# Performance work log

Hardware: AMD Instinct MI355X
Metric: run time of the kernel (lower is better)

Reference implementation:

```python
import jax, jax.numpy as jnp
import numpy as np

EPS_BN = 1e-5
EPS_NORM = 1e-12
TOP_K = 512


def _conv(x, w):
    # NCHW conv, stride 1, SAME padding (ultralytics Conv autopad)
    return jax.lax.conv_general_dilated(x, w, (1, 1), 'SAME',
                                        dimension_numbers=('NCHW', 'OIHW', 'NCHW'))


def _bn(x, g, b, m, v):
    # inference-mode BatchNorm2d
    inv = jax.lax.rsqrt(v + EPS_BN)
    return (x - m[None, :, None, None]) * (g * inv)[None, :, None, None] + b[None, :, None, None]


def _descriptor(feat, p):
    (w_dr, g_dr, b_dr, m_dr, v_dr,
     w_d1, g_d1, b_d1, m_d1, v_d1,
     g_e, b_e, m_e, v_e,
     w_d2, g_d2, b_d2, m_d2, v_d2) = p
    # dim_reduce: Conv(channel, channel//2, 1) = conv+BN+SiLU
    x = jax.nn.silu(_bn(_conv(feat, w_dr), g_dr, b_dr, m_dr, v_dr))
    # descriptor: Conv(c/2, c/2, 3) + BN + ReLU + Conv(c/2, c/4, 1)
    x = jax.nn.silu(_bn(_conv(x, w_d1), g_d1, b_d1, m_d1, v_d1))
    x = jax.nn.relu(_bn(x, g_e, b_e, m_e, v_e))
    x = jax.nn.silu(_bn(_conv(x, w_d2), g_d2, b_d2, m_d2, v_d2))
    return x


def _keypoints(desc):
    b, c, h, w = desc.shape
    resp = jnp.sqrt(jnp.sum(desc * desc, axis=1)).reshape(b, h * w)  # L2 norm over channels
    _, idx = jax.lax.top_k(resp, TOP_K)                              # [b, K]
    y = (idx // w).astype(desc.dtype) / (h - 1) * 2 - 1
    x = (idx % w).astype(desc.dtype) / (w - 1) * 2 - 1
    return jnp.stack([x, y], axis=-1), idx                           # [b,K,2], [b,K]


def _forward(rgb_feat, ir_feat, params):
    rgb_desc = _descriptor(rgb_feat, params)
    ir_desc = _descriptor(ir_feat, params)

    kp1, idx1 = _keypoints(rgb_desc)
    kp2, idx2 = _keypoints(ir_desc)

    b, c, h, w = rgb_desc.shape
    hw = h * w
    d1 = rgb_desc.reshape(b, c, hw)
    d2 = ir_desc.reshape(b, c, hw)
    d1 = d1 / jnp.maximum(jnp.linalg.norm(d1, axis=1, keepdims=True), EPS_NORM)
    d2 = d2 / jnp.maximum(jnp.linalg.norm(d2, axis=1, keepdims=True), EPS_NORM)
    corr = jnp.einsum('bcn,bcm->bnm', d1, d2)     # [b, hw, hw]
    soft = jax.nn.softmax(corr, axis=-1)

    # scalar matching weight per keypoint pair (gather at keypoint locations)
    bidx = jnp.arange(b)[:, None]
    wts = soft[bidx, idx1, idx2]                  # [b, K]

    # vectorized DLT: A rows, two per point, weighted
    x1, y1 = kp1[..., 0], kp1[..., 1]
    x2, y2 = kp2[..., 0], kp2[..., 1]
    one = jnp.ones_like(x1)
    zer = jnp.zeros_like(x1)
    r1 = jnp.stack([x1, y1, one, zer, zer, zer, -x2 * x1, -x2 * y1, -x2], axis=-1)
    r2 = jnp.stack([zer, zer, zer, x1, y1, one, -y2 * x1, -y2 * y1, -y2], axis=-1)
    A = jnp.stack([r1, r2], axis=2) * wts[:, :, None, None]   # [b,K,2,9]
    A = A.reshape(b, 2 * TOP_K, 9)

    _, _, Vh = jnp.linalg.svd(A, full_matrices=False)          # Vh: [b,9,9]
    # torch.svd returns V; original takes V[-1] == last COLUMN of jax Vh
    H = Vh[:, :, -1].reshape(b, 3, 3)
    return H, rgb_desc, ir_desc


def setup_inputs() -> dict:
    key = jax.random.key(0)
    ks = jax.random.split(key, 8)
    B, C, Hh, Ww = 2, 256, 64, 64
    c2, c4 = C // 2, C // 4
    f32 = jnp.float32

    def bn_params(c):
        return (jnp.ones((c,), f32), jnp.zeros((c,), f32),
                jnp.zeros((c,), f32), jnp.ones((c,), f32))

    g_dr, b_dr, m_dr, v_dr = bn_params(c2)
    g_d1, b_d1, m_d1, v_d1 = bn_params(c2)
    g_e, b_e, m_e, v_e = bn_params(c2)
    g_d2, b_d2, m_d2, v_d2 = bn_params(c4)

    return {
        'rgb_feat': jax.random.normal(ks[0], (B, C, Hh, Ww), f32),
        'ir_feat': jax.random.normal(ks[1], (B, C, Hh, Ww), f32),
        'w_dr': jax.random.normal(ks[2], (c2, C, 1, 1), f32) * 0.05,
        'g_dr': g_dr, 'b_dr': b_dr, 'm_dr': m_dr, 'v_dr': v_dr,
        'w_d1': jax.random.normal(ks[3], (c2, c2, 3, 3), f32) * 0.05,
        'g_d1': g_d1, 'b_d1': b_d1, 'm_d1': m_d1, 'v_d1': v_d1,
        'g_e': g_e, 'b_e': b_e, 'm_e': m_e, 'v_e': v_e,
        'w_d2': jax.random.normal(ks[4], (c4, c2, 1, 1), f32) * 0.05,
        'g_d2': g_d2, 'b_d2': b_d2, 'm_d2': m_d2, 'v_d2': v_d2,
    }


def reference(rgb_feat, ir_feat,
              w_dr, g_dr, b_dr, m_dr, v_dr,
              w_d1, g_d1, b_d1, m_d1, v_d1,
              g_e, b_e, m_e, v_e,
              w_d2, g_d2, b_d2, m_d2, v_d2):
    params = (w_dr, g_dr, b_dr, m_dr, v_dr,
              w_d1, g_d1, b_d1, m_d1, v_d1,
              g_e, b_e, m_e, v_e,
              w_d2, g_d2, b_d2, m_d2, v_d2)
    return _forward(rgb_feat, ir_feat, params)
```

## Files before the change

kernel.cpp:

```cpp
#include <hip/hip_runtime.h>
#include <math.h>


#define HW4 4096
#define NIMG 4

#define OFF_X1   0L
#define OFF_X2   (OFF_X1 + 4L*128*4096)
#define OFF_RESP (OFF_X2 + 4L*128*4096)
#define OFF_INVN (OFF_RESP + 4L*4096)
#define OFF_TOPI (OFF_INVN + 4L*4096)
#define OFF_WTS  (OFF_TOPI + 4L*512)
#define OFF_A    (OFF_WTS + 2L*512)
#define OFF_QN   OFF_X1
#define OFF_PART (OFF_X1 + 65536L)

#define NSPLIT 16

__device__ __forceinline__ float silu_f(float y) { return y / (1.f + expf(-y)); }

__global__ __launch_bounds__(256) void fm_conv1(
    const float* __restrict__ rgb, const float* __restrict__ ir,
    const float* __restrict__ w, const float* __restrict__ g,
    const float* __restrict__ bb, const float* __restrict__ mm,
    const float* __restrict__ vv, float* __restrict__ x1) {
  __shared__ float wl[256*8];
  int bid = blockIdx.x;
  int pblk = bid & 7, ocg = (bid >> 3) & 15, img = bid >> 7;
  int oc0 = ocg * 8;
  int tid = threadIdx.x;
  const float* src = (img < 2) ? (rgb + (long)img*256*HW4) : (ir + (long)(img-2)*256*HW4);
  for (int i = tid; i < 2048; i += 256) {
    int o = i & 7, ic = i >> 3;
    wl[i] = w[(oc0 + o)*256 + ic];
  }
  __syncthreads();
  int p0 = pblk*512 + tid*2;
  float acc[8][2];
  #pragma unroll
  for (int o = 0; o < 8; ++o) { acc[o][0] = 0.f; acc[o][1] = 0.f; }
  #pragma unroll 4
  for (int ic = 0; ic < 256; ++ic) {
    float2 v = *(const float2*)(src + (long)ic*HW4 + p0);
    float4 wa = *(const float4*)&wl[ic*8];
    float4 wb = *(const float4*)&wl[ic*8 + 4];
    acc[0][0] = fmaf(wa.x, v.x, acc[0][0]); acc[0][1] = fmaf(wa.x, v.y, acc[0][1]);
    acc[1][0] = fmaf(wa.y, v.x, acc[1][0]); acc[1][1] = fmaf(wa.y, v.y, acc[1][1]);
    acc[2][0] = fmaf(wa.z, v.x, acc[2][0]); acc[2][1] = fmaf(wa.z, v.y, acc[2][1]);
    acc[3][0] = fmaf(wa.w, v.x, acc[3][0]); acc[3][1] = fmaf(wa.w, v.y, acc[3][1]);
    acc[4][0] = fmaf(wb.x, v.x, acc[4][0]); acc[4][1] = fmaf(wb.x, v.y, acc[4][1]);
    acc[5][0] = fmaf(wb.y, v.x, acc[5][0]); acc[5][1] = fmaf(wb.y, v.y, acc[5][1]);
    acc[6][0] = fmaf(wb.z, v.x, acc[6][0]); acc[6][1] = fmaf(wb.z, v.y, acc[6][1]);
    acc[7][0] = fmaf(wb.w, v.x, acc[7][0]); acc[7][1] = fmaf(wb.w, v.y, acc[7][1]);
  }
  #pragma unroll
  for (int o = 0; o < 8; ++o) {
    int oc = oc0 + o;
    float inv = 1.f / sqrtf(vv[oc] + 1e-5f);
    float sc = g[oc]*inv;
    float2 r;
    r.x = silu_f((acc[o][0] - mm[oc])*sc + bb[oc]);
    r.y = silu_f((acc[o][1] - mm[oc])*sc + bb[oc]);
    *(float2*)(x1 + ((long)img*128 + oc)*HW4 + p0) = r;
  }
}

#define C3_TW 72
#define C3_TR 18
__global__ __launch_bounds__(256) void fm_conv3(
    const float* __restrict__ x1, const float* __restrict__ w,
    const float* __restrict__ g1, const float* __restrict__ b1,
    const float* __restrict__ m1, const float* __restrict__ v1,
    const float* __restrict__ ge, const float* __restrict__ be,
    const float* __restrict__ me, const float* __restrict__ ve,
    float* __restrict__ x2) {
  __shared__ float t[2][4][C3_TR*C3_TW];
  __shared__ float wl[2][4][9][4];
  int bid = blockIdx.x;
  int rt = bid & 3, ocg = (bid >> 2) & 31, img = bid >> 7;
  int oc0 = ocg * 4;
  int y0 = rt * 16;
  int tid = threadIdx.x;
  int ly = tid >> 4;
  int lx = tid & 15;
  int x0 = lx * 4;
  const float* xim = x1 + (long)img*128*HW4;

  int gbase[5][4];
  int lofs[5];
  #pragma unroll
  for (int t5 = 0; t5 < 5; ++t5) {
    int i = tid + 256*t5;
    if (i < 1224) {
      int q = i / 306, r = i - q*306;
      int row = r / 17, seg = r - row*17;
      int gy = y0 + row - 1;
      lofs[t5] = q*(C3_TR*C3_TW) + row*C3_TW + 4 + seg*4;
      #pragma unroll
      for (int e = 0; e < 4; ++e) {
        int x = seg*4 + e - 1;
        gbase[t5][e] = (gy >= 0 && gy < 64 && x >= 0 && x < 64)
                       ? (q*HW4 + gy*64 + x) : -1;
      }
    } else {
      lofs[t5] = -1;
      #pragma unroll
      for (int e = 0; e < 4; ++e) gbase[t5][e] = -1;
    }
  }
  int wg0 = -1, wl0 = 0;
  {
    int i = tid;
    if (i < 144) {
      int o = i & 3, k = (i >> 2) % 9, q = i / 36;
      wg0 = ((oc0 + o)*128 + q)*9 + k;
      wl0 = (q*9 + k)*4 + o;
    }
  }

  float4 sreg[5];
  float wreg0 = 0.f;

  #define C3_LOAD(IC0) do {                                              \
    long icoff = (long)(IC0)*HW4;                                        \
    _Pragma("unroll")                                                    \
    for (int t5 = 0; t5 < 5; ++t5) {                                     \
      sreg[t5].x = (gbase[t5][0] >= 0) ? xim[icoff + gbase[t5][0]] : 0.f;\
      sreg[t5].y = (gbase[t5][1] >= 0) ? xim[icoff + gbase[t5][1]] : 0.f;\
      sreg[t5].z = (gbase[t5][2] >= 0) ? xim[icoff + gbase[t5][2]] : 0.f;\
      sreg[t5].w = (gbase[t5][3] >= 0) ? xim[icoff + gbase[t5][3]] : 0.f;\
    }                                                                    \
    if (wg0 >= 0) wreg0 = w[(long)(IC0)*9 + wg0];                        \
  } while (0)

  #define C3_WRITE(BUF) do {                                             \
    float* tb = &t[BUF][0][0];                                           \
    _Pragma("unroll")                                                    \
    for (int t5 = 0; t5 < 5; ++t5)                                       \
      if (lofs[t5] >= 0) *(float4*)(tb + lofs[t5]) = sreg[t5];           \
    if (wg0 >= 0) (&wl[BUF][0][0][0])[wl0] = wreg0;                      \
  } while (0)

  float acc[4][4];
  #pragma unroll
  for (int o = 0; o < 4; ++o)
    #pragma unroll
    for (int j = 0; j < 4; ++j) acc[o][j] = 0.f;

  C3_LOAD(0);
  C3_WRITE(0);
  __syncthreads();
  int pb = 0;
  for (int ic0 = 0; ic0 < 128; ic0 += 4) {
    if (ic0 + 4 < 128) C3_LOAD(ic0 + 4);
    #pragma unroll
    for (int q = 0; q < 4; ++q) {
      const float* tq = &t[pb][q][0];
      float n6[3][6];
      #pragma unroll
      for (int dy = 0; dy < 3; ++dy) {
        float4 a = *(const float4*)(tq + (ly + dy)*C3_TW + x0 + 4);
        float4 b2 = *(const float4*)(tq + (ly + dy)*C3_TW + x0 + 8);
        n6[dy][0] = a.x; n6[dy][1] = a.y; n6[dy][2] = a.z;
        n6[dy][3] = a.w; n6[dy][4] = b2.x; n6[dy][5] = b2.y;
      }
      #pragma unroll
      for (int k = 0; k < 9; ++k) {
        const int dy = k / 3, dx = k % 3;
        float4 wA = *(const float4*)&wl[pb][q][k][0];
        #pragma unroll
        for (int j = 0; j < 4; ++j) {
          float nv = n6[dy][dx + j];
          acc[0][j] = fmaf(wA.x, nv, acc[0][j]);
          acc[1][j] = fmaf(wA.y, nv, acc[1][j]);
          acc[2][j] = fmaf(wA.z, nv, acc[2][j]);
          acc[3][j] = fmaf(wA.w, nv, acc[3][j]);
        }
      }
    }
    if (ic0 + 4 < 128) C3_WRITE(pb ^ 1);
    __syncthreads();
    pb ^= 1;
  }
  int prow = (y0 + ly)*64 + x0;
  #pragma unroll
  for (int o = 0; o < 4; ++o) {
    int oc = oc0 + o;
    float inv1 = 1.f / sqrtf(v1[oc] + 1e-5f);
    float s1 = g1[oc]*inv1;
    float inve = 1.f / sqrtf(ve[oc] + 1e-5f);
    float s2 = ge[oc]*inve;
    float4 r;
    float y;
    y = silu_f((acc[o][0] - m1[oc])*s1 + b1[oc]); r.x = fmaxf((y - me[oc])*s2 + be[oc], 0.f);
    y = silu_f((acc[o][1] - m1[oc])*s1 + b1[oc]); r.y = fmaxf((y - me[oc])*s2 + be[oc], 0.f);
    y = silu_f((acc[o][2] - m1[oc])*s1 + b1[oc]); r.z = fmaxf((y - me[oc])*s2 + be[oc], 0.f);
    y = silu_f((acc[o][3] - m1[oc])*s1 + b1[oc]); r.w = fmaxf((y - me[oc])*s2 + be[oc], 0.f);
    *(float4*)(x2 + ((long)img*128 + oc)*HW4 + prow) = r;
  }
}

__global__ __launch_bounds__(256) void fm_conv2(
    const float* __restrict__ x2, const float* __restrict__ w,
    const float* __restrict__ g, const float* __restrict__ bb,
    const float* __restrict__ mm, const float* __restrict__ vv,
    float* __restrict__ out) {
  __shared__ float wl[128*4];
  int bid = blockIdx.x;
  int pblk = bid & 7, ocg = (bid >> 3) & 15, img = bid >> 7;
  int oc0 = ocg * 4;
  int tid = threadIdx.x;
  for (int i = tid; i < 512; i += 256) {
    int o = i & 3, ic = i >> 2;
    wl[i] = w[(oc0 + o)*128 + ic];
  }
  __syncthreads();
  int p0 = pblk*512 + tid*2;
  const float* src = x2 + (long)img*128*HW4;
  float acc[4][2];
  #pragma unroll
  for (int o = 0; o < 4; ++o) { acc[o][0] = 0.f; acc[o][1] = 0.f; }
  #pragma unroll 4
  for (int ic = 0; ic < 128; ++ic) {
    float2 v = *(const float2*)(src + (long)ic*HW4 + p0);
    float4 wa = *(const float4*)&wl[ic*4];
    acc[0][0] = fmaf(wa.x, v.x, acc[0][0]); acc[0][1] = fmaf(wa.x, v.y, acc[0][1]);
    acc[1][0] = fmaf(wa.y, v.x, acc[1][0]); acc[1][1] = fmaf(wa.y, v.y, acc[1][1]);
    acc[2][0] = fmaf(wa.z, v.x, acc[2][0]); acc[2][1] = fmaf(wa.z, v.y, acc[2][1]);
    acc[3][0] = fmaf(wa.w, v.x, acc[3][0]); acc[3][1] = fmaf(wa.w, v.y, acc[3][1]);
  }
  #pragma unroll
  for (int o = 0; o < 4; ++o) {
    int oc = oc0 + o;
    float inv = 1.f / sqrtf(vv[oc] + 1e-5f);
    float sc = g[oc]*inv;
    float* dst = out + 18 + (long)img*262144 + (long)oc*HW4 + p0;
    dst[0] = silu_f((acc[o][0] - mm[oc])*sc + bb[oc]);
    dst[1] = silu_f((acc[o][1] - mm[oc])*sc + bb[oc]);
  }
}

__global__ __launch_bounds__(256) void fm_resp(
    const float* __restrict__ out, float* __restrict__ resp, float* __restrict__ invn) {
  int t = blockIdx.x*256 + threadIdx.x;
  if (t >= NIMG*HW4) return;
  int img = t >> 12, p = t & 4095;
  const float* d = out + 18 + (long)img*262144;
  float s = 0.f;
  #pragma unroll
  for (int c = 0; c < 64; ++c) { float x = d[c*HW4 + p]; s = fmaf(x, x, s); }
  float r = sqrtf(s);
  resp[t] = r;
  invn[t] = 1.f / fmaxf(r, 1e-12f);
}

__global__ __launch_bounds__(1024) void fm_sort(
    const float* __restrict__ resp, int* __restrict__ topidx) {
  __shared__ unsigned long long keys[4096];
  int img = blockIdx.x, tid = threadIdx.x;
  const float* r = resp + (long)img*HW4;
  for (int i = tid; i < 4096; i += 1024) {
    unsigned int vb = __float_as_uint(r[i]);
    keys[i] = ((unsigned long long)vb << 32) | (unsigned int)(4095 - i);
  }
  __syncthreads();
  for (int k = 2; k <= 4096; k <<= 1) {
    for (int j = k >> 1; j > 0; j >>= 1) {
      for (int t = tid; t < 2048; t += 1024) {
        int i = 2*t - (t & (j - 1));
        int ixj = i ^ j;
        bool up = ((i & k) == 0);
        unsigned long long a = keys[i], b = keys[ixj];
        if ((a < b) == up) { keys[i] = b; keys[ixj] = a; }
      }
      __syncthreads();
    }
  }
  if (tid < 512) topidx[img*512 + tid] = 4095 - (int)(keys[tid] & 0xFFFFFFFFull);
}

__global__ __launch_bounds__(256) void fm_qgather(
    const float* __restrict__ out, const float* __restrict__ invn,
    const int* __restrict__ topidx, float* __restrict__ qn) {
  int tid = threadIdx.x;
  int kp = blockIdx.x*4 + (tid >> 6);
  int c = tid & 63;
  int b = kp >> 9, k = kp & 511;
  int row = topidx[b*512 + k];
  const float* d1 = out + 18 + (long)b*262144;
  qn[(long)kp*64 + c] = d1[c*HW4 + row] * invn[(long)b*HW4 + row];
}

__global__ __launch_bounds__(256) void fm_corr(
    const float* __restrict__ out, const float* __restrict__ invn,
    const float* __restrict__ qn, float* __restrict__ part) {
  __shared__ float Qs[32*64];
  __shared__ float Ds[64*128];
  int tid = threadIdx.x;
  int tx = tid & 31, ty = tid >> 5;
  int jsplit = blockIdx.x;
  int kg = blockIdx.y;
  int b = blockIdx.z;
  int k0 = kg*32;
  const float* d2 = out + 18 + (long)(2 + b)*262144;
  const float* in2 = invn + (long)(2 + b)*HW4;
  {
    const float4* src = (const float4*)(qn + ((long)b*512 + k0)*64);
    float4* dst = (float4*)Qs;
    dst[tid] = src[tid];
    dst[tid + 256] = src[tid + 256];
  }
  float m[4], s[4];
  #pragma unroll
  for (int r = 0; r < 4; ++r) { m[r] = -INFINITY; s[r] = 0.f; }
  #pragma unroll
  for (int tile = 0; tile < 2; ++tile) {
    int j0 = jsplit*256 + tile*128;
    __syncthreads();
    {
      float4* dst = (float4*)Ds;
      #pragma unroll
      for (int t = 0; t < 8; ++t) {
        int i = tid + 256*t;
        int c = i >> 5, col4 = i & 31;
        dst[i] = *(const float4*)(d2 + (long)c*HW4 + j0 + col4*4);
      }
    }
    __syncthreads();
    float acc[4][4];
    #pragma unroll
    for (int r = 0; r < 4; ++r)
      #pragma unroll
      for (int cc = 0; cc < 4; ++cc) acc[r][cc] = 0.f;
    const float4* Ds4 = (const float4*)Ds;
    #pragma unroll 4
    for (int c = 0; c < 64; ++c) {
      float4 dv = Ds4[c*32 + tx];
      #pragma unroll
      for (int r = 0; r < 4; ++r) {
        float qv = Qs[(ty*4 + r)*64 + c];
        acc[r][0] = fmaf(qv, dv.x, acc[r][0]);
        acc[r][1] = fmaf(qv, dv.y, acc[r][1]);
        acc[r][2] = fmaf(qv, dv.z, acc[r][2]);
        acc[r][3] = fmaf(qv, dv.w, acc[r][3]);
      }
    }
    float i0 = in2[j0 + tx*4 + 0];
    float i1 = in2[j0 + tx*4 + 1];
    float i2 = in2[j0 + tx*4 + 2];
    float i3 = in2[j0 + tx*4 + 3];
    #pragma unroll
    for (int r = 0; r < 4; ++r) {
      float v0 = acc[r][0]*i0, v1 = acc[r][1]*i1, v2 = acc[r][2]*i2, v3 = acc[r][3]*i3;
      float vm = fmaxf(fmaxf(v0, v1), fmaxf(v2, v3));
      float nm = fmaxf(m[r], vm);
      s[r] = s[r]*expf(m[r] - nm) + expf(v0 - nm) + expf(v1 - nm) + expf(v2 - nm) + expf(v3 - nm);
      m[r] = nm;
    }
  }
  #pragma unroll
  for (int off = 1; off < 32; off <<= 1) {
    #pragma unroll
    for (int r = 0; r < 4; ++r) {
      float om = __shfl_xor(m[r], off);
      float os = __shfl_xor(s[r], off);
      float nm = fmaxf(m[r], om);
      s[r] = s[r]*expf(m[r] - nm) + os*expf(om - nm);
      m[r] = nm;
    }
  }
  if (tx == 0) {
    #pragma unroll
    for (int r = 0; r < 4; ++r) {
      long idx = (((long)b*512 + k0 + ty*4 + r)*NSPLIT + jsplit)*2;
      part[idx] = m[r];
      part[idx + 1] = s[r];
    }
  }
}

__global__ __launch_bounds__(256) void fm_comb(
    const float* __restrict__ out, const float* __restrict__ invn,
    const int* __restrict__ topidx, const float* __restrict__ qn,
    const float* __restrict__ part, float* __restrict__ wts) {
  int tid = threadIdx.x;
  int kp = blockIdx.x*4 + (tid >> 6);
  int lane = tid & 63;
  int b = kp >> 9, k = kp & 511;
  int col = topidx[(2 + b)*512 + k];
  const float* d2 = out + 18 + (long)(2 + b)*262144;
  float dot = qn[(long)kp*64 + lane] * d2[lane*HW4 + col];
  #pragma unroll
  for (int off = 1; off < 64; off <<= 1) dot += __shfl_xor(dot, off);
  if (lane == 0) {
    const float* pp = part + (long)kp*NSPLIT*2;
    float M = -INFINITY;
    #pragma unroll
    for (int i = 0; i < NSPLIT; ++i) M = fmaxf(M, pp[2*i]);
    float S = 0.f;
    #pragma unroll
    for (int i = 0; i < NSPLIT; ++i) S += pp[2*i + 1]*expf(pp[2*i] - M);
    float v = dot * invn[(long)(2 + b)*HW4 + col];
    wts[b*512 + k] = expf(v - M)/S;
  }
}

__global__ __launch_bounds__(256) void fm_build(
    const int* __restrict__ topidx, const float* __restrict__ wts,
    float* __restrict__ A) {
  int t = blockIdx.x*256 + threadIdx.x;
  if (t >= 1024) return;
  int b = t >> 9, k = t & 511;
  int i1 = topidx[b*512 + k], i2 = topidx[(2 + b)*512 + k];
  float w = wts[b*512 + k];
  float x1 = (float)(i1 & 63) / 63.f * 2.f - 1.f;
  float y1 = (float)(i1 >> 6) / 63.f * 2.f - 1.f;
  float x2 = (float)(i2 & 63) / 63.f * 2.f - 1.f;
  float y2 = (float)(i2 >> 6) / 63.f * 2.f - 1.f;
  float* r = A + ((long)b*1024 + 2*k)*9;
  r[0] = x1*w;  r[1] = y1*w;  r[2] = w;
  r[3] = 0.f;   r[4] = 0.f;   r[5] = 0.f;
  r[6] = (-x2*x1)*w; r[7] = (-x2*y1)*w; r[8] = (-x2)*w;
  r[9]  = 0.f;  r[10] = 0.f;  r[11] = 0.f;
  r[12] = x1*w; r[13] = y1*w; r[14] = w;
  r[15] = (-y2*x1)*w; r[16] = (-y2*y1)*w; r[17] = (-y2)*w;
}

__device__ __forceinline__ void lap_slartg(float f, float g, float* cs, float* sn, float* r) {
  if (g == 0.f) { *cs = 1.f; *sn = 0.f; *r = f; }
  else if (f == 0.f) { *cs = 0.f; *sn = copysignf(1.f, g); *r = fabsf(g); }
  else {
    float d = sqrtf(f*f + g*g);
    *cs = fabsf(f) / d;
    *r = copysignf(d, f);
    *sn = g / (*r);
  }
}

__device__ __forceinline__ void lap_slas2(float f, float g, float h, float* ssmin, float* ssmax) {
  float fa = fabsf(f), ga = fabsf(g), ha = fabsf(h);
  float fhmn = fminf(fa, ha), fhmx = fmaxf(fa, ha);
  if (fhmn == 0.f) {
    *ssmin = 0.f;
    if (fhmx == 0.f) *ssmax = ga;
    else {
      float mx = fmaxf(fhmx, ga), mn = fminf(fhmx, ga);
      float q = mn / mx;
      *ssmax = mx * sqrtf(1.f + q*q);
    }
  } else {
    if (ga < fhmx) {
      float as_ = 1.f + fhmn/fhmx;
      float at_ = (fhmx - fhmn)/fhmx;
      float au = ga/fhmx; au = au*au;
      float c = 2.f / (sqrtf(as_*as_ + au) + sqrtf(at_*at_ + au));
      *ssmin = fhmn*c;
      *ssmax = fhmx/c;
    } else {
      float au = fhmx/ga;
      if (au == 0.f) { *ssmin = (fhmn*fhmx)/ga; *ssmax = ga; }
      else {
        float as_ = 1.f + fhmn/fhmx;
        float at_ = (fhmx - fhmn)/fhmx;
        float t1 = as_*au, t2 = at_*au;
        float c = 1.f / (sqrtf(1.f + t1*t1) + sqrtf(1.f + t2*t2));
        float smn = (fhmn*c)*au;
        *ssmin = smn + smn;
        *ssmax = ga/(c + c);
      }
    }
  }
}

__device__ __forceinline__ void lap_slasv2(float f, float g, float h, float* ssmin, float* ssmax,
                           float* snr, float* csr, float* snl, float* csl) {
  const float epsv = 5.9604645e-08f;
  float ft = f, fa = fabsf(f), ht = h, ha = fabsf(h);
  int pmax = 1;
  bool swap_ = (ha > fa);
  if (swap_) { pmax = 3; float tmp = ft; ft = ht; ht = tmp; tmp = fa; fa = ha; ha = tmp; }
  float gt = g, ga = fabsf(gt);
  float clt = 0.f, crt = 0.f, slt = 0.f, srt = 0.f;
  if (ga == 0.f) { *ssmin = ha; *ssmax = fa; clt = 1.f; crt = 1.f; slt = 0.f; srt = 0.f; }
  else {
    bool gasmal = true;
    if (ga > fa) {
      pmax = 2;
      if ((fa/ga) < epsv) {
        gasmal = false;
        *ssmax = ga;
        if (ha > 1.f) *ssmin = fa/(ga/ha); else *ssmin = (fa/ga)*ha;
        clt = 1.f; slt = ht/gt; srt = 1.f; crt = ft/gt;
      }
    }
    if (gasmal) {
      float d = fa - ha, l;
      if (d == fa) l = 1.f; else l = d/fa;
      float m_ = gt/ft;
      float t = 2.f - l;
      float mm2 = m_*m_, tt = t*t;
      float s = sqrtf(tt + mm2);
      float r_ = (l == 0.f) ? fabsf(m_) : sqrtf(l*l + mm2);
      float a = 0.5f*(s + r_);
      *ssmin = ha/a;
      *ssmax = fa*a;
      if (mm2 == 0.f) {
        if (l == 0.f) t = copysignf(2.f, ft)*copysignf(1.f, gt);
        else t = gt/copysignf(d, ft) + m_/t;
      } else {
        t = (m_/(s + t) + m_/(r_ + l))*(1.f + a);
      }
      float l2 = sqrtf(t*t + 4.f);
      crt = 2.f/l2;
      srt = t/l2;
      clt = (crt + srt*m_)/a;
      slt = (ht/ft)*srt/a;
    }
  }
  if (swap_) { *csl = srt; *snl = crt; *csr = slt; *snr = clt; }
  else { *csl = clt; *snl = slt; *csr = crt; *snr = srt; }
  float tsign = 1.f;
  if (pmax == 1) tsign = copysignf(1.f, *csr)*copysignf(1.f, *csl)*copysignf(1.f, f);
  if (pmax == 2) tsign = copysignf(1.f, *snr)*copysignf(1.f, *csl)*copysignf(1.f, g);
  if (pmax == 3) tsign = copysignf(1.f, *snr)*copysignf(1.f, *snl)*copysignf(1.f, h);
  *ssmax = copysignf(*ssmax, tsign);
  *ssmin = copysignf(*ssmin, tsign*copysignf(1.f, f)*copysignf(1.f, h));
}

__device__ __forceinline__ float get9(const float (&a)[9], int idx) {
  float v = a[0];
#pragma unroll
  for (int i = 1; i < 9; ++i) if (idx == i) v = a[i];
  return v;
}
__device__ __forceinline__ void set9(float (&a)[9], int idx, float val) {
#pragma unroll
  for (int i = 0; i < 9; ++i) if (idx == i) a[i] = val;
}

__device__ __forceinline__ void bdsqr9_reg(float (&dd)[9], float (&ee)[9], float (&vt)[9]) {
  const float eps_ = 5.9604645e-08f;
  const float unfl_ = 1.17549435e-38f;
  const float tol_ = 10.f*eps_;
  float sminoa = fabsf(dd[0]);
  if (sminoa != 0.f) {
    float mu = sminoa;
    bool z = false;
#pragma unroll
    for (int i = 1; i < 9; ++i) {
      if (!z) {
        mu = fabsf(dd[i])*(mu/(mu + fabsf(ee[i-1])));
        sminoa = fminf(sminoa, mu);
        if (sminoa == 0.f) z = true;
      }
    }
  }
  sminoa = sminoa / 3.f;
  float thresh = fmaxf(tol_*sminoa, 486.f*unfl_);
  int m = 9, iter = 0, oldll = -1, oldm = -1, idir = 0;
  float sminl = 0.f;
  int guard = 0;
  while (guard++ < 2000) {
    if (m <= 1) break;
    if (iter > 486) break;
    float smax = fabsf(get9(dd, m-1));
    int ll = 0; bool split = false;
#pragma unroll
    for (int l2 = 8; l2 >= 1; --l2) {
      if (l2 <= m - 1 && !split) {
        float abss = fabsf(dd[l2-1]);
        float abse = fabsf(ee[l2-1]);
        if (abse <= thresh) { ll = l2; split = true; }
        else smax = fmaxf(smax, fmaxf(abss, abse));
      }
    }
    if (split) {
      set9(ee, ll-1, 0.f);
      if (ll == m - 1) { m = m - 1; continue; }
    } else ll = 0;
    ll = ll + 1;
    if (ll == m - 1) {
      float d1 = get9(dd, m-2), e1 = get9(ee, m-2), d2v = get9(dd, m-1);
      float sigmn, sigmx, sinr, cosr, sinl_, cosl_;
      lap_slasv2(d1, e1, d2v, &sigmn, &sigmx, &sinr, &cosr, &sinl_, &cosl_);
      set9(dd, m-2, sigmx); set9(ee, m-2, 0.f); set9(dd, m-1, sigmn);
      float xt = get9(vt, m-2), yt = get9(vt, m-1);
      set9(vt, m-2, cosr*xt + sinr*yt);
      set9(vt, m-1, cosr*yt - sinr*xt);
      m -= 2; continue;
    }
    if (ll > oldm || m < oldll)
      idir = (fabsf(get9(dd, ll-1)) >= fabsf(get9(dd, m-1))) ? 1 : 2;
    bool conv = false;
    if (idir == 1) {
      if (fabsf(get9(ee, m-2)) <= tol_*fabsf(get9(dd, m-1))) { set9(ee, m-2, 0.f); continue; }
      float mu = fabsf(get9(dd, ll-1));
      sminl = mu;
#pragma unroll
      for (int lll = 1; lll <= 8; ++lll) {
        if (lll >= ll && lll <= m - 1 && !conv) {
          if (fabsf(ee[lll-1]) <= tol_*mu) { ee[lll-1] = 0.f; conv = true; }
          else {
            mu = fabsf(dd[lll])*(mu/(mu + fabsf(ee[lll-1])));
            sminl = fminf(sminl, mu);
          }
        }
      }
    } else {
      if (fabsf(get9(ee, ll-1)) <= tol_*fabsf(get9(dd, ll-1))) { set9(ee, ll-1, 0.f); continue; }
      float mu = fabsf(get9(dd, m-1));
      sminl = mu;
#pragma unroll
      for (int lll = 8; lll >= 1; --lll) {
        if (lll <= m - 1 && lll >= ll && !conv) {
          if (fabsf(ee[lll-1]) <= tol_*mu) { ee[lll-1] = 0.f; conv = true; }
          else {
            mu = fabsf(dd[lll-1])*(mu/(mu + fabsf(ee[lll-1])));
            sminl = fminf(sminl, mu);
          }
        }
      }
    }
    if (conv) continue;
    oldll = ll; oldm = m;
    float shift = 0.f, rdum;
    if (!(9.f*tol_*(sminl/smax) <= fmaxf(eps_, 0.01f*tol_))) {
      float sll;
      if (idir == 1) { sll = fabsf(get9(dd, ll-1)); lap_slas2(get9(dd, m-2), get9(ee, m-2), get9(dd, m-1), &shift, &rdum); }
      else           { sll = fabsf(get9(dd, m-1));  lap_slas2(get9(dd, ll-1), get9(ee, ll-1), get9(dd, ll), &shift, &rdum); }
      if (sll > 0.f) { float q = shift/sll; if (q*q < eps_) shift = 0.f; }
    }
    iter += m - ll;
    if (shift == 0.f) {
      if (idir == 1) {
        float cs = 1.f, oldcs = 1.f, sn = 0.f, oldsn = 0.f, r;
#pragma unroll
        for (int i = 1; i <= 8; ++i) {
          if (i >= ll && i <= m - 1) {
            lap_slartg(dd[i-1]*cs, ee[i-1], &cs, &sn, &r);
            if (i >= 2 && i > ll) ee[i-2] = oldsn*r;
            float dn;
            lap_slartg(oldcs*r, dd[i]*sn, &oldcs, &oldsn, &dn);
            dd[i-1] = dn;
            float t = vt[i]; vt[i] = cs*t - sn*vt[i-1]; vt[i-1] = sn*t + cs*vt[i-1];
          }
        }
        float h2 = get9(dd, m-1)*cs;
        set9(dd, m-1, h2*oldcs);
        set9(ee, m-2, h2*oldsn);
        if (fabsf(get9(ee, m-2)) <= thresh) set9(ee, m-2, 0.f);
      } else {
        float cs = 1.f, oldcs = 1.f, sn = 0.f, oldsn = 0.f, r;
#pragma unroll
        for (int i = 9; i >= 2; --i) {
          if (i <= m && i >= ll + 1) {
            lap_slartg(dd[i-1]*cs, ee[i-2], &cs, &sn, &r);
            if (i < m) ee[i-1] = oldsn*r;
            float dn;
            lap_slartg(oldcs*r, dd[i-2]*sn, &oldcs, &oldsn, &dn);
            dd[i-1] = dn;
            float c2 = oldcs, s2 = -oldsn;
            float t = vt[i-1]; vt[i-1] = c2*t - s2*vt[i-2]; vt[i-2] = s2*t + c2*vt[i-2];
          }
        }
        float h2 = get9(dd, ll-1)*cs;
        set9(dd, ll-1, h2*oldcs);
        set9(ee, ll-1, h2*oldsn);
        if (fabsf(get9(ee, ll-1)) <= thresh) set9(ee, ll-1, 0.f);
      }
    } else {
      if (idir == 1) {
        float d0 = get9(dd, ll-1);
        float f2 = (fabsf(d0) - shift)*(copysignf(1.f, d0) + shift/d0);
        float g2 = get9(ee, ll-1);
#pragma unroll
        for (int i = 1; i <= 8; ++i) {
          if (i >= ll && i <= m - 1) {
            float cr, sr, cl, sl, r;
            lap_slartg(f2, g2, &cr, &sr, &r);
            if (i >= 2 && i > ll) ee[i-2] = r;
            f2 = cr*dd[i-1] + sr*ee[i-1];
            ee[i-1] = cr*ee[i-1] - sr*dd[i-1];
            g2 = sr*dd[i];
            dd[i] = cr*dd[i];
            lap_slartg(f2, g2, &cl, &sl, &r);
            dd[i-1] = r;
            f2 = cl*ee[i-1] + sl*dd[i];
            dd[i] = cl*dd[i] - sl*ee[i-1];
            if (i < m - 1) { g2 = sl*ee[i]; ee[i] = cl*ee[i]; }
            float t = vt[i]; vt[i] = cr*t - sr*vt[i-1]; vt[i-1] = sr*t + cr*vt[i-1];
          }
        }
        set9(ee, m-2, f2);
        if (fabsf(get9(ee, m-2)) <= thresh) set9(ee, m-2, 0.f);
      } else {
        float dm = get9(dd, m-1);
        float f2 = (fabsf(dm) - shift)*(copysignf(1.f, dm) + shift/dm);
        float g2 = get9(ee, m-2);
#pragma unroll
        for (int i = 9; i >= 2; --i) {
          if (i <= m && i >= ll + 1) {
            float cr, sr, cl, sl, r;
            lap_slartg(f2, g2, &cr, &sr, &r);
            if (i < m) ee[i-1] = r;
            f2 = cr*dd[i-1] + sr*ee[i-2];
            ee[i-2] = cr*ee[i-2] - sr*dd[i-1];
            g2 = sr*dd[i-2];
            dd[i-2] = cr*dd[i-2];
            lap_slartg(f2, g2, &cl, &sl, &r);
            dd[i-1] = r;
            f2 = cl*ee[i-2] + sl*dd[i-2];
            dd[i-2] = cl*dd[i-2] - sl*ee[i-2];
            if (i >= 3 && i > ll + 1) { g2 = sl*ee[i-3]; ee[i-3] = cl*ee[i-3]; }
            float c2 = cl, s2 = -sl;
            float t = vt[i-1]; vt[i-1] = c2*t - s2*vt[i-2]; vt[i-2] = s2*t + c2*vt[i-2];
          }
        }
        set9(ee, ll-1, f2);
        if (fabsf(get9(ee, ll-1)) <= thresh) set9(ee, ll-1, 0.f);
      }
    }
  }
#pragma unroll
  for (int i = 0; i < 9; ++i) {
    if (dd[i] < 0.f) { dd[i] = -dd[i]; vt[i] = -vt[i]; }
  }
#pragma unroll
  for (int i = 1; i <= 8; ++i) {
    int isub = 1; float smin2 = dd[0];
#pragma unroll
    for (int j = 2; j <= 9; ++j) {
      if (j <= 10 - i) {
        if (dd[j-1] <= smin2) { isub = j; smin2 = dd[j-1]; }
      }
    }
    const int tgt = 10 - i;
    if (isub != tgt) {
      set9(dd, isub-1, dd[tgt-1]);
      dd[tgt-1] = smin2;
      float tv = get9(vt, isub-1);
      set9(vt, isub-1, vt[tgt-1]);
      vt[tgt-1] = tv;
    }
  }
}

__global__ __launch_bounds__(256) void fm_svd(
    const float* __restrict__ Aglob, float* __restrict__ outH) {
  __shared__ float As[1024*9];
  __shared__ float wred[4][12];
  __shared__ float bc[4];
  int b = blockIdx.x, tid = threadIdx.x;
  int wv = tid >> 6, ln = tid & 63;
  const float* Ab = Aglob + (long)b*9216;
  {
    const float4* s4 = (const float4*)Ab;
    float4* d4 = (float4*)As;
#pragma unroll
    for (int t = 0; t < 9; ++t) d4[tid + 256*t] = s4[tid + 256*t];
  }
  __syncthreads();
  for (int k = 0; k < 9; ++k) {
    float ps = 0.f;
    for (int r = k + 1 + tid; r < 1024; r += 256) {
      float x = As[r*9 + k]; ps = fmaf(x, x, ps);
    }
#pragma unroll
    for (int off = 1; off < 64; off <<= 1) ps += __shfl_xor(ps, off);
    if (ln == 0) wred[wv][8] = ps;
    __syncthreads();
    if (tid == 0) {
      float ssq = wred[0][8] + wred[1][8] + wred[2][8] + wred[3][8];
      float alpha = As[k*9 + k];
      float tau = 0.f, sc = 0.f, beta = alpha;
      if (ssq != 0.f) {
        beta = -copysignf(sqrtf(alpha*alpha + ssq), alpha);
        tau = (beta - alpha)/beta;
        sc = 1.f/(alpha - beta);
      }
      bc[0] = tau; bc[1] = sc; bc[2] = beta;
    }
    __syncthreads();
    float tau = bc[0], sc = bc[1];
    if (tau != 0.f) {
      for (int r = k + 1 + tid; r < 1024; r += 256) As[r*9 + k] *= sc;
    }
    __syncthreads();
    if (tau != 0.f) {
      float pd[8];
#pragma unroll
      for (int jj = 0; jj < 8; ++jj) pd[jj] = 0.f;
      for (int r = k + 1 + tid; r < 1024; r += 256) {
        float vk = As[r*9 + k];
#pragma unroll
        for (int jj = 0; jj < 8; ++jj) {
          int j = k + 1 + jj;
          if (j < 9) pd[jj] = fmaf(vk, As[r*9 + j], pd[jj]);
        }
      }
#pragma unroll
      for (int off = 1; off < 64; off <<= 1) {
#pragma unroll
        for (int jj = 0; jj < 8; ++jj) pd[jj] += __shfl_xor(pd[jj], off);
      }
      if (ln == 0) {
#pragma unroll
        for (int jj = 0; jj < 8; ++jj) wred[wv][jj] = pd[jj];
      }
      __syncthreads();
      float sj[8];
#pragma unroll
      for (int jj = 0; jj < 8; ++jj) {
        int j = k + 1 + jj;
        float v = 0.f;
        if (j < 9)
          v = (wred[0][jj] + wred[1][jj] + wred[2][jj] + wred[3][jj] + As[k*9 + j]) * tau;
        sj[jj] = v;
      }
      for (int r = k + 1 + tid; r < 1024; r += 256) {
        float vk = As[r*9 + k];
#pragma unroll
        for (int jj = 0; jj < 8; ++jj) {
          int j = k + 1 + jj;
          if (j < 9) As[r*9 + j] -= sj[jj]*vk;
        }
      }
      __syncthreads();
      if (tid == 0) {
#pragma unroll
        for (int jj = 0; jj < 8; ++jj) {
          int j = k + 1 + jj;
          if (j < 9) As[k*9 + j] -= sj[jj];
        }
      }
    }
    if (tid == 0) As[k*9 + k] = bc[2];
    __syncthreads();
  }
  if (tid < 64) {
    float R[9][9];
#pragma unroll
    for (int i = 0; i < 9; ++i)
#pragma unroll
      for (int j = 0; j < 9; ++j)
        R[i][j] = (j >= i) ? As[i*9 + j] : 0.f;
    float dd[9], ee[9], taupv[8], pt8[9];
    ee[8] = 0.f;
#pragma unroll
    for (int i = 0; i < 9; ++i) {
      float alpha = R[i][i];
      float ssq = 0.f;
#pragma unroll
      for (int r2 = i + 1; r2 < 9; ++r2) ssq += R[r2][i]*R[r2][i];
      float tauq = 0.f, beta = alpha;
      if (ssq != 0.f) {
        beta = -copysignf(sqrtf(alpha*alpha + ssq), alpha);
        tauq = (beta - alpha)/beta;
        float scq = 1.f/(alpha - beta);
#pragma unroll
        for (int r2 = i + 1; r2 < 9; ++r2) R[r2][i] *= scq;
      }
      dd[i] = beta;
      if (tauq != 0.f) {
#pragma unroll
        for (int j = i + 1; j < 9; ++j) {
          float s = R[i][j];
#pragma unroll
          for (int r2 = i + 1; r2 < 9; ++r2) s += R[r2][i]*R[r2][j];
          s *= tauq;
          R[i][j] -= s;
#pragma unroll
          for (int r2 = i + 1; r2 < 9; ++r2) R[r2][j] -= s*R[r2][i];
        }
      }
      if (i < 8) {
        float alpha2 = R[i][i+1];
        float ssq2 = 0.f;
#pragma unroll
        for (int c = i + 2; c < 9; ++c) ssq2 += R[i][c]*R[i][c];
        float tp = 0.f, beta2 = alpha2;
        if (ssq2 != 0.f) {
          beta2 = -copysignf(sqrtf(alpha2*alpha2 + ssq2), alpha2);
          tp = (beta2 - alpha2)/beta2;
          float scp = 1.f/(alpha2 - beta2);
#pragma unroll
          for (int c = i + 2; c < 9; ++c) R[i][c] *= scp;
        }
        ee[i] = beta2;
        taupv[i] = tp;
        if (tp != 0.f) {
#pragma unroll
          for (int r2 = i + 1; r2 < 9; ++r2) {
            float s = R[r2][i+1];
#pragma unroll
            for (int c = i + 2; c < 9; ++c) s += R[i][c]*R[r2][c];
            s *= tp;
            R[r2][i+1] -= s;
#pragma unroll
            for (int c = i + 2; c < 9; ++c) R[r2][c] -= s*R[i][c];
          }
        }
      }
    }
#pragma unroll
    for (int i = 0; i < 9; ++i) pt8[i] = (i == 8) ? 1.f : 0.f;
#pragma unroll
    for (int i = 0; i < 8; ++i) {
      float tp = taupv[i];
      if (tp != 0.f) {
        float s = pt8[i+1];
#pragma unroll
        for (int r2 = i + 2; r2 < 9; ++r2) s += R[i][r2]*pt8[r2];
        s *= tp;
        pt8[i+1] -= s;
#pragma unroll
        for (int r2 = i + 2; r2 < 9; ++r2) pt8[r2] -= s*R[i][r2];
      }
    }
    float vt[9];
#pragma unroll
    for (int i = 0; i < 9; ++i) vt[i] = (i == tid) ? 1.f : 0.f;
    bdsqr9_reg(dd, ee, vt);
    float p8 = (tid < 9) ? get9(pt8, tid) : 0.f;
    float h[9];
#pragma unroll
    for (int i = 0; i < 9; ++i) h[i] = vt[i]*p8;
#pragma unroll
    for (int off = 1; off < 16; off <<= 1) {
#pragma unroll
      for (int i = 0; i < 9; ++i) h[i] += __shfl_xor(h[i], off);
    }
    if (tid == 0) {
#pragma unroll
      for (int i = 0; i < 9; ++i) outH[b*9 + i] = h[i];
    }
  }
}

extern "C" void kernel_launch(void* const* d_in, const int* in_sizes, int n_in,
                              void* d_out, int out_size, void* d_ws, size_t ws_size,
                              hipStream_t stream) {
  const float* rgb  = (const float*)d_in[0];
  const float* ir   = (const float*)d_in[1];
  const float* w_dr = (const float*)d_in[2];
  const float* g_dr = (const float*)d_in[3];
  const float* b_dr = (const float*)d_in[4];
  const float* m_dr = (const float*)d_in[5];
  const float* v_dr = (const float*)d_in[6];
  const float* w_d1 = (const float*)d_in[7];
  const float* g_d1 = (const float*)d_in[8];
  const float* b_d1 = (const float*)d_in[9];
  const float* m_d1 = (const float*)d_in[10];
  const float* v_d1 = (const float*)d_in[11];
  const float* g_e  = (const float*)d_in[12];
  const float* b_e  = (const float*)d_in[13];
  const float* m_e  = (const float*)d_in[14];
  const float* v_e  = (const float*)d_in[15];
  const float* w_d2 = (const float*)d_in[16];
  const float* g_d2 = (const float*)d_in[17];
  const float* b_d2 = (const float*)d_in[18];
  const float* m_d2 = (const float*)d_in[19];
  const float* v_d2 = (const float*)d_in[20];

  float* out = (float*)d_out;
  float* ws  = (float*)d_ws;
  float* x1   = ws + OFF_X1;
  float* x2   = ws + OFF_X2;
  float* resp = ws + OFF_RESP;
  float* invn = ws + OFF_INVN;
  int*   topi = (int*)(ws + OFF_TOPI);
  float* wts  = ws + OFF_WTS;
  float* Amat = ws + OFF_A;
  float* qn   = ws + OFF_QN;
  float* part = ws + OFF_PART;

  fm_conv1<<<512, 256, 0, stream>>>(rgb, ir, w_dr, g_dr, b_dr, m_dr, v_dr, x1);
  fm_conv3<<<512, 256, 0, stream>>>(x1, w_d1, g_d1, b_d1, m_d1, v_d1,
                                    g_e, b_e, m_e, v_e, x2);
  fm_conv2<<<512, 256, 0, stream>>>(x2, w_d2, g_d2, b_d2, m_d2, v_d2, out);
  fm_resp<<<(NIMG*HW4 + 255)/256, 256, 0, stream>>>(out, resp, invn);
  fm_sort<<<NIMG, 1024, 0, stream>>>(resp, topi);
  fm_qgather<<<256, 256, 0, stream>>>(out, invn, topi, qn);
  fm_corr<<<dim3(NSPLIT, 16, 2), 256, 0, stream>>>(out, invn, qn, part);
  fm_comb<<<256, 256, 0, stream>>>(out, invn, topi, qn, part, wts);
  fm_build<<<4, 256, 0, stream>>>(topi, wts, Amat);
  fm_svd<<<2, 256, 0, stream>>>(Amat, out);
}
```

Measured before the change: 412.2 us.

## Compute eight output channels per block in 3x3 conv, read weights directly

The 3x3 conv kernel now computes 8 output channels per block instead of 4, halving the grid to 256 blocks. Each input tile staged in shared memory is reused across twice as many outputs, so input traffic drops. Weights are no longer staged in LDS; they are read straight from global memory with uniform addresses, which should become scalar loads. The cost is more registers (32 accumulators plus 72 neighbourhood values) and fewer blocks, which may lower occupancy and leave CUs idle.

```diff
diff --git a/kernel.cpp b/kernel.cpp
--- a/kernel.cpp
+++ b/kernel.cpp
@@ -75,10 +75,9 @@
     const float* __restrict__ me, const float* __restrict__ ve,
     float* __restrict__ x2) {
   __shared__ float t[2][4][C3_TR*C3_TW];
-  __shared__ float wl[2][4][9][4];
   int bid = blockIdx.x;
-  int rt = bid & 3, ocg = (bid >> 2) & 31, img = bid >> 7;
-  int oc0 = ocg * 4;
+  int rt = bid & 3, ocg = (bid >> 2) & 15, img = bid >> 6;
+  int oc0 = ocg * 8;
   int y0 = rt * 16;
   int tid = threadIdx.x;
   int ly = tid >> 4;
@@ -108,18 +107,8 @@
       for (int e = 0; e < 4; ++e) gbase[t5][e] = -1;
     }
   }
-  int wg0 = -1, wl0 = 0;
-  {
-    int i = tid;
-    if (i < 144) {
-      int o = i & 3, k = (i >> 2) % 9, q = i / 36;
-      wg0 = ((oc0 + o)*128 + q)*9 + k;
-      wl0 = (q*9 + k)*4 + o;
-    }
-  }
 
   float4 sreg[5];
-  float wreg0 = 0.f;
 
   #define C3_LOAD(IC0) do {                                              \
     long icoff = (long)(IC0)*HW4;                                        \
@@ -130,7 +119,6 @@
       sreg[t5].z = (gbase[t5][2] >= 0) ? xim[icoff + gbase[t5][2]] : 0.f;\
       sreg[t5].w = (gbase[t5][3] >= 0) ? xim[icoff + gbase[t5][3]] : 0.f;\
     }                                                                    \
-    if (wg0 >= 0) wreg0 = w[(long)(IC0)*9 + wg0];                        \
   } while (0)
 
   #define C3_WRITE(BUF) do {                                             \
@@ -138,12 +126,11 @@
     _Pragma("unroll")                                                    \
     for (int t5 = 0; t5 < 5; ++t5)                                       \
       if (lofs[t5] >= 0) *(float4*)(tb + lofs[t5]) = sreg[t5];           \
-    if (wg0 >= 0) (&wl[BUF][0][0][0])[wl0] = wreg0;                      \
   } while (0)
 
-  float acc[4][4];
-  #pragma unroll
-  for (int o = 0; o < 4; ++o)
+  float acc[8][4];
+  #pragma unroll
+  for (int o = 0; o < 8; ++o)
     #pragma unroll
     for (int j = 0; j < 4; ++j) acc[o][j] = 0.f;
 
@@ -153,28 +140,31 @@
   int pb = 0;
   for (int ic0 = 0; ic0 < 128; ic0 += 4) {
     if (ic0 + 4 < 128) C3_LOAD(ic0 + 4);
+    float n6[4][3][6];
     #pragma unroll
     for (int q = 0; q < 4; ++q) {
       const float* tq = &t[pb][q][0];
-      float n6[3][6];
       #pragma unroll
       for (int dy = 0; dy < 3; ++dy) {
         float4 a = *(const float4*)(tq + (ly + dy)*C3_TW + x0 + 4);
         float4 b2 = *(const float4*)(tq + (ly + dy)*C3_TW + x0 + 8);
-        n6[dy][0] = a.x; n6[dy][1] = a.y; n6[dy][2] = a.z;
-        n6[dy][3] = a.w; n6[dy][4] = b2.x; n6[dy][5] = b2.y;
-      }
+        n6[q][dy][0] = a.x; n6[q][dy][1] = a.y; n6[q][dy][2] = a.z;
+        n6[q][dy][3] = a.w; n6[q][dy][4] = b2.x; n6[q][dy][5] = b2.y;
+      }
+    }
+    const float* wbase = w + ((long)oc0*128 + ic0)*9;
+    #pragma unroll
+    for (int o = 0; o < 8; ++o) {
+      const float* wo = wbase + (long)o*1152;
       #pragma unroll
-      for (int k = 0; k < 9; ++k) {
-        const int dy = k / 3, dx = k % 3;
-        float4 wA = *(const float4*)&wl[pb][q][k][0];
+      for (int q = 0; q < 4; ++q) {
         #pragma unroll
-        for (int j = 0; j < 4; ++j) {
-          float nv = n6[dy][dx + j];
-          acc[0][j] = fmaf(wA.x, nv, acc[0][j]);
-          acc[1][j] = fmaf(wA.y, nv, acc[1][j]);
-          acc[2][j] = fmaf(wA.z, nv, acc[2][j]);
-          acc[3][j] = fmaf(wA.w, nv, acc[3][j]);
+        for (int k = 0; k < 9; ++k) {
+          float wv = wo[q*9 + k];
+          const int dy = k / 3, dx = k - dy*3;
+          #pragma unroll
+          for (int j = 0; j < 4; ++j)
+            acc[o][j] = fmaf(wv, n6[q][dy][dx + j], acc[o][j]);
         }
       }
     }
@@ -184,7 +174,7 @@
   }
   int prow = (y0 + ly)*64 + x0;
   #pragma unroll
-  for (int o = 0; o < 4; ++o) {
+  for (int o = 0; o < 8; ++o) {
     int oc = oc0 + o;
     float inv1 = 1.f / sqrtf(v1[oc] + 1e-5f);
     float s1 = g1[oc]*inv1;
@@ -975,7 +965,7 @@
   float* part = ws + OFF_PART;
 
   fm_conv1<<<512, 256, 0, stream>>>(rgb, ir, w_dr, g_dr, b_dr, m_dr, v_dr, x1);
-  fm_conv3<<<512, 256, 0, stream>>>(x1, w_d1, g_d1, b_d1, m_d1, v_d1,
+  fm_conv3<<<256, 256, 0, stream>>>(x1, w_d1, g_d1, b_d1, m_d1, v_d1,
                                     g_e, b_e, m_e, v_e, x2);
   fm_conv2<<<512, 256, 0, stream>>>(x2, w_d2, g_d2, b_d2, m_d2, v_d2, out);
   fm_resp<<<(NIMG*HW4 + 255)/256, 256, 0, stream>>>(out, resp, invn);
```

After: 487.6 us. +18.3%, slower.
